# Kernel tuning notes

Hardware: AMD Instinct MI355X
Metric: run time of the kernel (lower is better)

## Reference

```python
import jax, jax.numpy as jnp
import numpy as np

D_MODEL = 1024
NUM_HEADS = 16
D_K = D_MODEL // NUM_HEADS


def setup_inputs() -> dict:
    key = jax.random.key(0)
    ks = jax.random.split(key, 11)
    B, S, D = 4, 2048, D_MODEL
    scale = 1.0 / np.sqrt(D)
    return {
        "Q": jax.random.normal(ks[0], (B, S, D), jnp.float32),
        "K": jax.random.normal(ks[1], (B, S, D), jnp.float32),
        "V": jax.random.normal(ks[2], (B, S, D), jnp.float32),
        "Wq": jax.random.normal(ks[3], (D, D), jnp.float32) * scale,
        "bq": jnp.zeros((D,), jnp.float32),
        "Wk": jax.random.normal(ks[4], (D, D), jnp.float32) * scale,
        "bk": jnp.zeros((D,), jnp.float32),
        "Wv": jax.random.normal(ks[5], (D, D), jnp.float32) * scale,
        "bv": jnp.zeros((D,), jnp.float32),
        "Wo": jax.random.normal(ks[6], (D, D), jnp.float32) * scale,
        "bo": jnp.zeros((D,), jnp.float32),
    }


def reference(Q, K, V, Wq, bq, Wk, bk, Wv, bv, Wo, bo):
    B, S, D = Q.shape
    H, Dk = NUM_HEADS, D_K
    # projections: [B,S,D] -> [B,H,S,Dk]
    def proj(x, W, b):
        y = jnp.einsum('bsd,de->bse', x, W.T) + b  # torch Linear: x @ W.T + b
        return y.reshape(B, -1, H, Dk).transpose(0, 2, 1, 3)
    q = proj(Q, Wq, bq)
    k = proj(K, Wk, bk)
    v = proj(V, Wv, bv)
    scores = jnp.einsum('bhqd,bhkd->bhqk', q, k) / np.sqrt(Dk)  # [B,H,S,S]
    attn = jax.nn.softmax(scores, axis=-1)
    out = jnp.einsum('bhqk,bhkd->bhqd', attn, v)  # [B,H,S,Dk]
    out = out.transpose(0, 2, 1, 3).reshape(B, -1, D)
    return jnp.einsum('bsd,de->bse', out, Wo.T) + bo
```

## Files before the change

kernel.cpp:

```cpp
#include <hip/hip_runtime.h>


typedef __bf16 bhalf_t;
typedef __attribute__((ext_vector_type(8)))  __bf16 bf16x8;
typedef __attribute__((ext_vector_type(4)))  __bf16 bf16x4;
typedef __attribute__((ext_vector_type(4)))  float  f32x4;
typedef __attribute__((ext_vector_type(16))) float  f32x16;

typedef __attribute__((address_space(1))) void gvoid_t;
typedef __attribute__((address_space(3))) void lvoid_t;
#define GLD16(g, l) __builtin_amdgcn_global_load_lds((const gvoid_t*)(g), (lvoid_t*)(l), 16, 0, 0)

__global__ __launch_bounds__(256) void cvt_all(
    const float* __restrict__ Q, const float* __restrict__ Kin, const float* __restrict__ V,
    const float* __restrict__ Wq, const float* __restrict__ Wk, const float* __restrict__ Wv,
    const float* __restrict__ Wo,
    bhalf_t* __restrict__ Qb, bhalf_t* __restrict__ Kb, bhalf_t* __restrict__ Vb,
    bhalf_t* __restrict__ Wqb, bhalf_t* __restrict__ Wkb, bhalf_t* __restrict__ Wvb,
    bhalf_t* __restrict__ Wob)
{
  size_t t = (size_t)blockIdx.x * 256 + threadIdx.x;
  const float* src; bhalf_t* dst;
  if (t < 2097152)      { src = Q;   dst = Qb; }
  else if (t < 4194304) { src = Kin; dst = Kb; t -= 2097152; }
  else if (t < 6291456) { src = V;   dst = Vb; t -= 4194304; }
  else {
    t -= 6291456;
    int w = (int)(t >> 18); t &= 262143;
    src = (w == 0) ? Wq  : (w == 1) ? Wk  : (w == 2) ? Wv  : Wo;
    dst = (w == 0) ? Wqb : (w == 1) ? Wkb : (w == 2) ? Wvb : Wob;
  }
  float4 f = ((const float4*)src)[t];
  bf16x4 o;
  o.x = (bhalf_t)f.x; o.y = (bhalf_t)f.y; o.z = (bhalf_t)f.z; o.w = (bhalf_t)f.w;
  ((bf16x4*)dst)[t] = o;
}

__device__ __forceinline__ void gemm_core_128(
    const bhalf_t* __restrict__ A, const bhalf_t* __restrict__ B,
    int bm, int bn, bhalf_t* As, bhalf_t* Bs, f32x4 acc[4][4])
{
  const int tid = threadIdx.x, lane = tid & 63, wave = tid >> 6;
  const int wm = wave >> 1, wn = wave & 1;
  const int quad = lane >> 4, tn = lane & 15;
  const int srow = lane >> 2, scol = (lane & 3) * 8;

  const bhalf_t* Ab0 = A + (size_t)(bm * 128 + wave * 16 + srow) * 1024 + scol;
  const bhalf_t* Ab1 = Ab0 + (size_t)64 * 1024;
  const bhalf_t* Bb0 = B + (size_t)(bn * 128 + wave * 16 + srow) * 1024 + scol;
  const bhalf_t* Bb1 = Bb0 + (size_t)64 * 1024;
  bhalf_t* Asw0 = As + wave * 512;  bhalf_t* Asw1 = As + (wave + 4) * 512;
  bhalf_t* Bsw0 = Bs + wave * 512;  bhalf_t* Bsw1 = Bs + (wave + 4) * 512;

  for (int k0 = 0; k0 < 1024; k0 += 32) {
    GLD16(Ab0 + k0, Asw0);
    GLD16(Ab1 + k0, Asw1);
    GLD16(Bb0 + k0, Bsw0);
    GLD16(Bb1 + k0, Bsw1);
    __syncthreads();
    bf16x8 af[4], bfr[4];
#pragma unroll
    for (int i = 0; i < 4; ++i)
      af[i] = *(const bf16x8*)(As + (wm * 64 + i * 16 + tn) * 32 + quad * 8);
#pragma unroll
    for (int j = 0; j < 4; ++j)
      bfr[j] = *(const bf16x8*)(Bs + (wn * 64 + j * 16 + tn) * 32 + quad * 8);
#pragma unroll
    for (int i = 0; i < 4; ++i)
#pragma unroll
      for (int j = 0; j < 4; ++j)
        acc[i][j] = __builtin_amdgcn_mfma_f32_16x16x32_bf16(af[i], bfr[j], acc[i][j], 0, 0, 0);
    __syncthreads();
  }
}

__global__ __launch_bounds__(256) void proj_gemm(
    const bhalf_t* __restrict__ Qb, const bhalf_t* __restrict__ Kb, const bhalf_t* __restrict__ Vb,
    const bhalf_t* __restrict__ Wqb, const bhalf_t* __restrict__ Wkb, const bhalf_t* __restrict__ Wvb,
    const float* __restrict__ bq, const float* __restrict__ bk, const float* __restrict__ bv,
    bhalf_t* __restrict__ qo, bhalf_t* __restrict__ ko, bhalf_t* __restrict__ vto)
{
  __shared__ bhalf_t As[4096];
  __shared__ bhalf_t Bs[4096];
  const int seg = blockIdx.x >> 9;
  const int idx = blockIdx.x & 511;
  const int bm = idx & 63, bn = idx >> 6;

  const bhalf_t *A, *Bw; const float* bias; bhalf_t* out; float scale; int mode;
  if (seg == 0)      { A = Qb; Bw = Wqb; bias = bq; out = qo;  scale = 0.18033688f; mode = 0; }
  else if (seg == 1) { A = Kb; Bw = Wkb; bias = bk; out = ko;  scale = 1.0f;        mode = 0; }
  else               { A = Vb; Bw = Wvb; bias = bv; out = vto; scale = 1.0f;        mode = 1; }

  f32x4 acc[4][4];
#pragma unroll
  for (int i = 0; i < 4; ++i)
#pragma unroll
    for (int j = 0; j < 4; ++j)
      acc[i][j] = (f32x4){0.f, 0.f, 0.f, 0.f};

  gemm_core_128(A, Bw, bm, bn, As, Bs, acc);

  const int lane = threadIdx.x & 63, wave = threadIdx.x >> 6;
  const int wm = wave >> 1, wn = wave & 1, quad = lane >> 4, tn = lane & 15;
#pragma unroll
  for (int i = 0; i < 4; ++i)
#pragma unroll
    for (int j = 0; j < 4; ++j) {
      const int n = bn * 128 + wn * 64 + j * 16 + tn;
      const float bsv = bias[n];
      const int h = n >> 6, dk = n & 63;
#pragma unroll
      for (int r = 0; r < 4; ++r) {
        const int m = bm * 128 + wm * 64 + i * 16 + quad * 4 + r;
        const int b = m >> 11, s = m & 2047;
        const float v = (acc[i][j][r] + bsv) * scale;
        size_t addr;
        if (mode == 0) addr = (((size_t)(b * 16 + h)) * 2048 + s) * 64 + dk;
        else {
          const int s2 = (s & ~12) | ((s & 4) << 1) | ((s & 8) >> 1);
          addr = (((size_t)(b * 16 + h)) * 64 + dk) * 2048 + s2;
        }
        out[addr] = (bhalf_t)v;
      }
    }
}

__global__ __launch_bounds__(256) void out_gemm(
    const bhalf_t* __restrict__ A, const bhalf_t* __restrict__ Bw,
    const float* __restrict__ bias, float* __restrict__ Cout)
{
  __shared__ bhalf_t As[4096];
  __shared__ bhalf_t Bs[4096];
  const int bm = blockIdx.x & 63, bn = blockIdx.x >> 6;

  f32x4 acc[4][4];
#pragma unroll
  for (int i = 0; i < 4; ++i)
#pragma unroll
    for (int j = 0; j < 4; ++j)
      acc[i][j] = (f32x4){0.f, 0.f, 0.f, 0.f};

  gemm_core_128(A, Bw, bm, bn, As, Bs, acc);

  const int lane = threadIdx.x & 63, wave = threadIdx.x >> 6;
  const int wm = wave >> 1, wn = wave & 1, quad = lane >> 4, tn = lane & 15;
#pragma unroll
  for (int i = 0; i < 4; ++i)
#pragma unroll
    for (int j = 0; j < 4; ++j) {
      const int n = bn * 128 + wn * 64 + j * 16 + tn;
      const float bsv = bias[n];
#pragma unroll
      for (int r = 0; r < 4; ++r) {
        const int m = bm * 128 + wm * 64 + i * 16 + quad * 4 + r;
        Cout[(size_t)m * 1024 + n] = acc[i][j][r] + bsv;
      }
    }
}

__global__ __launch_bounds__(256, 2) void attn_kernel(
    const bhalf_t* __restrict__ qp, const bhalf_t* __restrict__ kp,
    const bhalf_t* __restrict__ vtp, bhalf_t* __restrict__ outp)
{
  __shared__ bhalf_t Klds[4096];
  __shared__ bhalf_t Vtlds[4096];

  const int tid = threadIdx.x, lane = tid & 63, wave = tid >> 6;
  const int q31 = lane & 31, h = lane >> 5;
  const int bh = blockIdx.y, qt = blockIdx.x;

  const bhalf_t* qbase = qp + (((size_t)bh * 2048) + qt * 256 + wave * 64 + q31) * 64;
  bf16x8 qf[2][4];
#pragma unroll
  for (int qs = 0; qs < 2; ++qs)
#pragma unroll
    for (int ks = 0; ks < 4; ++ks)
      qf[qs][ks] = *(const bf16x8*)(qbase + qs * 32 * 64 + ks * 16 + h * 8);

  f32x16 Ot[2][2];
#pragma unroll
  for (int qs = 0; qs < 2; ++qs)
#pragma unroll
    for (int dd = 0; dd < 2; ++dd)
#pragma unroll
      for (int i = 0; i < 16; ++i) Ot[qs][dd][i] = 0.f;
  float Lp[2] = {0.f, 0.f};

  const bhalf_t* kbase  = kp  + (size_t)bh * 2048 * 64;
  const bhalf_t* vtbase = vtp + (size_t)bh * 64 * 2048;

  const int rloc = lane >> 3;
  const int cg8  = ((lane & 7) ^ rloc) * 8;
  const int q7 = q31 & 7;

  for (int kv0 = 0; kv0 < 2048; kv0 += 64) {
#pragma unroll
    for (int i = 0; i < 2; ++i) {
      const int r0 = (wave * 2 + i) * 8;
      GLD16(kbase + (size_t)(kv0 + r0 + rloc) * 64 + cg8, Klds + r0 * 64);
      GLD16(vtbase + (size_t)(r0 + rloc) * 2048 + kv0 + cg8, Vtlds + r0 * 64);
    }
    __syncthreads();

    bf16x8 pb[2][4];
#pragma unroll
    for (int mb = 0; mb < 2; ++mb) {
      bf16x8 ka[4];
#pragma unroll
      for (int ks = 0; ks < 4; ++ks)
        ka[ks] = *(const bf16x8*)(Klds + (mb * 32 + q31) * 64 + ((2 * ks + h) ^ q7) * 8);
#pragma unroll
      for (int qs = 0; qs < 2; ++qs) {
        f32x16 S;
#pragma unroll
        for (int i = 0; i < 16; ++i) S[i] = 0.f;
#pragma unroll
        for (int ks = 0; ks < 4; ++ks)
          S = __builtin_amdgcn_mfma_f32_32x32x16_bf16(ka[ks], qf[qs][ks], S, 0, 0, 0);
        float ls = 0.f;
#pragma unroll
        for (int half = 0; half < 2; ++half) {
          bf16x8 pk;
#pragma unroll
          for (int j = 0; j < 8; ++j) {
            const float e = __builtin_amdgcn_exp2f(S[half * 8 + j]);
            ls += e;
            pk[j] = (bhalf_t)e;
          }
          pb[qs][mb * 2 + half] = pk;
        }
        Lp[qs] += ls;
      }
    }

#pragma unroll
    for (int dd = 0; dd < 2; ++dd)
#pragma unroll
      for (int kb = 0; kb < 4; ++kb) {
        const bf16x8 va = *(const bf16x8*)(Vtlds + (dd * 32 + q31) * 64 + ((2 * kb + h) ^ q7) * 8);
#pragma unroll
        for (int qs = 0; qs < 2; ++qs)
          Ot[qs][dd] = __builtin_amdgcn_mfma_f32_32x32x16_bf16(va, pb[qs][kb], Ot[qs][dd], 0, 0, 0);
      }
    __syncthreads();
  }

  const int b = bh >> 4, hh = bh & 15;
#pragma unroll
  for (int qs = 0; qs < 2; ++qs) {
    const float Lt = Lp[qs] + __shfl_xor(Lp[qs], 32, 64);
    const float linv = 1.0f / Lt;
    const int s = qt * 256 + wave * 64 + qs * 32 + q31;
    bhalf_t* ob = outp + ((size_t)(b * 2048 + s)) * 1024 + hh * 64;
#pragma unroll
    for (int dd = 0; dd < 2; ++dd)
#pragma unroll
      for (int g = 0; g < 4; ++g) {
        bf16x4 o;
        o.x = (bhalf_t)(Ot[qs][dd][4 * g + 0] * linv);
        o.y = (bhalf_t)(Ot[qs][dd][4 * g + 1] * linv);
        o.z = (bhalf_t)(Ot[qs][dd][4 * g + 2] * linv);
        o.w = (bhalf_t)(Ot[qs][dd][4 * g + 3] * linv);
        *(bf16x4*)(ob + dd * 32 + g * 8 + h * 4) = o;
      }
  }
}

extern "C" void kernel_launch(void* const* d_in, const int* in_sizes, int n_in,
                              void* d_out, int out_size, void* d_ws, size_t ws_size,
                              hipStream_t stream)
{
  const float* Q  = (const float*)d_in[0];
  const float* K  = (const float*)d_in[1];
  const float* V  = (const float*)d_in[2];
  const float* Wq = (const float*)d_in[3];
  const float* bq = (const float*)d_in[4];
  const float* Wk = (const float*)d_in[5];
  const float* bk = (const float*)d_in[6];
  const float* Wv = (const float*)d_in[7];
  const float* bv = (const float*)d_in[8];
  const float* Wo = (const float*)d_in[9];
  const float* bo = (const float*)d_in[10];

  char* ws = (char*)d_ws;
  const size_t SZ = 8192ull * 1024 * 2;
  const size_t WZ = 1024ull * 1024 * 2;
  bhalf_t* Qb   = (bhalf_t*)(ws);
  bhalf_t* Kb   = (bhalf_t*)(ws + SZ);
  bhalf_t* Vb   = (bhalf_t*)(ws + 2 * SZ);
  bhalf_t* Wqb  = (bhalf_t*)(ws + 3 * SZ);
  bhalf_t* Wkb  = (bhalf_t*)(ws + 3 * SZ + WZ);
  bhalf_t* Wvb  = (bhalf_t*)(ws + 3 * SZ + 2 * WZ);
  bhalf_t* Wob  = (bhalf_t*)(ws + 3 * SZ + 3 * WZ);
  bhalf_t* q_p  = (bhalf_t*)(ws + 3 * SZ + 4 * WZ);
  bhalf_t* k_p  = (bhalf_t*)(ws + 4 * SZ + 4 * WZ);
  bhalf_t* vt_p = (bhalf_t*)(ws + 5 * SZ + 4 * WZ);
  bhalf_t* attn_o = Qb;

  cvt_all<<<28672, 256, 0, stream>>>(Q, K, V, Wq, Wk, Wv, Wo,
                                     Qb, Kb, Vb, Wqb, Wkb, Wvb, Wob);
  proj_gemm<<<1536, 256, 0, stream>>>(Qb, Kb, Vb, Wqb, Wkb, Wvb,
                                      bq, bk, bv, q_p, k_p, vt_p);
  attn_kernel<<<dim3(8, 64), 256, 0, stream>>>(q_p, k_p, vt_p, attn_o);
  out_gemm<<<512, 256, 0, stream>>>(attn_o, Wob, bo, (float*)d_out);
}
```

Baseline: 336.6 us.

## Rewrite projection GEMM as 256x256 tile with 4-stage async LDS pipeline

```diff
diff --git a/kernel.cpp b/kernel.cpp
--- a/kernel.cpp
+++ b/kernel.cpp
@@ -10,6 +10,11 @@
 typedef __attribute__((address_space(1))) void gvoid_t;
 typedef __attribute__((address_space(3))) void lvoid_t;
 #define GLD16(g, l) __builtin_amdgcn_global_load_lds((const gvoid_t*)(g), (lvoid_t*)(l), 16, 0, 0)
+
+#define SB0()   __builtin_amdgcn_sched_barrier(0)
+#define BARX()  asm volatile("s_barrier" ::: "memory")
+#define LGKM0() asm volatile("s_waitcnt lgkmcnt(0)" ::: "memory")
+#define VMW(n)  asm volatile("s_waitcnt vmcnt(" #n ")" ::: "memory")
 
 __global__ __launch_bounds__(256) void cvt_all(
     const float* __restrict__ Q, const float* __restrict__ Kin, const float* __restrict__ V,
@@ -74,44 +79,125 @@
   }
 }
 
-__global__ __launch_bounds__(256) void proj_gemm(
+#define PROJ_ITER(T, ISSUE, GATE)                                              \
+  {                                                                            \
+    bhalf_t* AsB = As + ((T) & 3) * 8192;                                      \
+    bhalf_t* BsB = Bs + ((T) & 3) * 8192;                                      \
+    bf16x8 af[4], bg[4];                                                       \
+    _Pragma("unroll")                                                          \
+    for (int i = 0; i < 4; ++i)                                                \
+      af[i] = *(const bf16x8*)(AsB + arow + i * 1024 + aswz);                  \
+    _Pragma("unroll")                                                          \
+    for (int j = 0; j < 4; ++j)                                                \
+      bg[j] = *(const bf16x8*)(BsB + brow + j * 1024 + bswz);                  \
+    if (ISSUE) {                                                               \
+      bhalf_t* And = As + (((T) + 3) & 3) * 8192;                              \
+      GLD16(Asrc0 + ((T) + 3) * 32, And + w * 512);                            \
+      GLD16(Asrc1 + ((T) + 3) * 32, And + (w + 8) * 512);                      \
+    }                                                                          \
+    BARX(); LGKM0(); SB0();                                                    \
+    __builtin_amdgcn_s_setprio(1);                                             \
+    _Pragma("unroll")                                                          \
+    for (int i = 0; i < 4; ++i)                                                \
+      _Pragma("unroll")                                                        \
+      for (int j = 0; j < 4; ++j)                                              \
+        acc[i][j] = __builtin_amdgcn_mfma_f32_16x16x32_bf16(af[i], bg[j], acc[i][j], 0, 0, 0); \
+    __builtin_amdgcn_s_setprio(0); SB0();                                      \
+    BARX();                                                                    \
+    _Pragma("unroll")                                                          \
+    for (int i = 0; i < 4; ++i)                                                \
+      af[i] = *(const bf16x8*)(AsB + arow + (i + 4) * 1024 + aswz);            \
+    if (ISSUE) {                                                               \
+      bhalf_t* Bnd = Bs + (((T) + 3) & 3) * 8192;                              \
+      GLD16(Bsrc0 + ((T) + 3) * 32, Bnd + w * 512);                            \
+      GLD16(Bsrc1 + ((T) + 3) * 32, Bnd + (w + 8) * 512);                      \
+    }                                                                          \
+    BARX(); LGKM0(); SB0();                                                    \
+    __builtin_amdgcn_s_setprio(1);                                             \
+    _Pragma("unroll")                                                          \
+    for (int i = 0; i < 4; ++i)                                                \
+      _Pragma("unroll")                                                        \
+      for (int j = 0; j < 4; ++j)                                              \
+        acc[i + 4][j] = __builtin_amdgcn_mfma_f32_16x16x32_bf16(af[i], bg[j], acc[i + 4][j], 0, 0, 0); \
+    __builtin_amdgcn_s_setprio(0); SB0();                                      \
+    GATE; SB0();                                                               \
+    BARX();                                                                    \
+  }
+
+__global__ __launch_bounds__(512, 2) void proj_gemm(
     const bhalf_t* __restrict__ Qb, const bhalf_t* __restrict__ Kb, const bhalf_t* __restrict__ Vb,
     const bhalf_t* __restrict__ Wqb, const bhalf_t* __restrict__ Wkb, const bhalf_t* __restrict__ Wvb,
     const float* __restrict__ bq, const float* __restrict__ bk, const float* __restrict__ bv,
     bhalf_t* __restrict__ qo, bhalf_t* __restrict__ ko, bhalf_t* __restrict__ vto)
 {
-  __shared__ bhalf_t As[4096];
-  __shared__ bhalf_t Bs[4096];
-  const int seg = blockIdx.x >> 9;
-  const int idx = blockIdx.x & 511;
-  const int bm = idx & 63, bn = idx >> 6;
+  __shared__ bhalf_t As[4 * 8192];
+  __shared__ bhalf_t Bs[4 * 8192];
+
+  const int bid = blockIdx.x;
+  const int wg = (bid & 7) * 48 + (bid >> 3);
+  const int seg = wg >> 7;
+  const int idx = wg & 127;
+  const int bm = idx >> 2, bn = idx & 3;
 
   const bhalf_t *A, *Bw; const float* bias; bhalf_t* out; float scale; int mode;
   if (seg == 0)      { A = Qb; Bw = Wqb; bias = bq; out = qo;  scale = 0.18033688f; mode = 0; }
   else if (seg == 1) { A = Kb; Bw = Wkb; bias = bk; out = ko;  scale = 1.0f;        mode = 0; }
   else               { A = Vb; Bw = Wvb; bias = bv; out = vto; scale = 1.0f;        mode = 1; }
 
-  f32x4 acc[4][4];
-#pragma unroll
-  for (int i = 0; i < 4; ++i)
+  const int tid = threadIdx.x, lane = tid & 63, w = tid >> 6;
+  const int wm = w >> 2, wn = w & 3;
+  const int quad = lane >> 4, tn = lane & 15;
+
+  const int c    = (lane & 7) ^ ((lane >> 3) & 7);
+  const int rA   = w * 8 + (lane >> 3);
+  const int grow = rA + 128 * (c >> 2);
+  const int kcol = (c & 3) * 8;
+  const bhalf_t* Asrc0 = A  + (size_t)(bm * 256 + grow) * 1024 + kcol;
+  const bhalf_t* Asrc1 = Asrc0 + (size_t)64 * 1024;
+  const bhalf_t* Bsrc0 = Bw + (size_t)(bn * 256 + grow) * 1024 + kcol;
+  const bhalf_t* Bsrc1 = Bsrc0 + (size_t)64 * 1024;
+
+  const int aswz = (((wm << 2) | quad) ^ (tn & 7)) * 8;
+  const int bswz = ((((wn >> 1) << 2) | quad) ^ (tn & 7)) * 8;
+  const int arow = tn * 64;
+  const int brow = (((wn & 1) << 6) + tn) * 64;
+
+  f32x4 acc[8][4];
+#pragma unroll
+  for (int i = 0; i < 8; ++i)
 #pragma unroll
     for (int j = 0; j < 4; ++j)
       acc[i][j] = (f32x4){0.f, 0.f, 0.f, 0.f};
 
-  gemm_core_128(A, Bw, bm, bn, As, Bs, acc);
-
-  const int lane = threadIdx.x & 63, wave = threadIdx.x >> 6;
-  const int wm = wave >> 1, wn = wave & 1, quad = lane >> 4, tn = lane & 15;
-#pragma unroll
-  for (int i = 0; i < 4; ++i)
+#pragma unroll
+  for (int t = 0; t < 3; ++t) {
+    bhalf_t* And = As + t * 8192;
+    bhalf_t* Bnd = Bs + t * 8192;
+    GLD16(Asrc0 + t * 32, And + w * 512);
+    GLD16(Asrc1 + t * 32, And + (w + 8) * 512);
+    GLD16(Bsrc0 + t * 32, Bnd + w * 512);
+    GLD16(Bsrc1 + t * 32, Bnd + (w + 8) * 512);
+  }
+  VMW(8); SB0();
+  BARX();
+
+#pragma unroll 4
+  for (int t = 0; t < 28; ++t) PROJ_ITER(t, true, VMW(8));
+  PROJ_ITER(28, true,  VMW(8));
+  PROJ_ITER(29, false, VMW(4));
+  PROJ_ITER(30, false, VMW(0));
+  PROJ_ITER(31, false, (void)0);
+
+#pragma unroll
+  for (int i = 0; i < 8; ++i)
 #pragma unroll
     for (int j = 0; j < 4; ++j) {
-      const int n = bn * 128 + wn * 64 + j * 16 + tn;
+      const int n = bn * 256 + wn * 64 + j * 16 + tn;
       const float bsv = bias[n];
       const int h = n >> 6, dk = n & 63;
 #pragma unroll
       for (int r = 0; r < 4; ++r) {
-        const int m = bm * 128 + wm * 64 + i * 16 + quad * 4 + r;
+        const int m = bm * 256 + wm * 128 + i * 16 + quad * 4 + r;
         const int b = m >> 11, s = m & 2047;
         const float v = (acc[i][j][r] + bsv) * scale;
         size_t addr;
@@ -299,8 +385,8 @@
 
   cvt_all<<<28672, 256, 0, stream>>>(Q, K, V, Wq, Wk, Wv, Wo,
                                      Qb, Kb, Vb, Wqb, Wkb, Wvb, Wob);
-  proj_gemm<<<1536, 256, 0, stream>>>(Qb, Kb, Vb, Wqb, Wkb, Wvb,
-                                      bq, bk, bv, q_p, k_p, vt_p);
+  proj_gemm<<<384, 512, 0, stream>>>(Qb, Kb, Vb, Wqb, Wkb, Wvb,
+                                     bq, bk, bv, q_p, k_p, vt_p);
   attn_kernel<<<dim3(8, 64), 256, 0, stream>>>(q_p, k_p, vt_p, attn_o);
   out_gemm<<<512, 256, 0, stream>>>(attn_o, Wob, bo, (float*)d_out);
 }
```

Result: slower. 366.3 us (+8.8%).

## Fuse fp32-to-bf16 activation conversion into projection GEMM and swizzle LDS tiles

Applied to the files above, without the earlier changes.

```diff
diff --git a/kernel.cpp b/kernel.cpp
--- a/kernel.cpp
+++ b/kernel.cpp
@@ -11,60 +11,57 @@
 typedef __attribute__((address_space(3))) void lvoid_t;
 #define GLD16(g, l) __builtin_amdgcn_global_load_lds((const gvoid_t*)(g), (lvoid_t*)(l), 16, 0, 0)
 
-__global__ __launch_bounds__(256) void cvt_all(
-    const float* __restrict__ Q, const float* __restrict__ Kin, const float* __restrict__ V,
-    const float* __restrict__ Wq, const float* __restrict__ Wk, const float* __restrict__ Wv,
-    const float* __restrict__ Wo,
-    bhalf_t* __restrict__ Qb, bhalf_t* __restrict__ Kb, bhalf_t* __restrict__ Vb,
-    bhalf_t* __restrict__ Wqb, bhalf_t* __restrict__ Wkb, bhalf_t* __restrict__ Wvb,
-    bhalf_t* __restrict__ Wob)
+__global__ __launch_bounds__(256) void cvt_w(
+    const float* __restrict__ Wq, const float* __restrict__ Wk,
+    const float* __restrict__ Wv, const float* __restrict__ Wo,
+    bhalf_t* __restrict__ Wqb, bhalf_t* __restrict__ Wkb,
+    bhalf_t* __restrict__ Wvb, bhalf_t* __restrict__ Wob)
 {
   size_t t = (size_t)blockIdx.x * 256 + threadIdx.x;
-  const float* src; bhalf_t* dst;
-  if (t < 2097152)      { src = Q;   dst = Qb; }
-  else if (t < 4194304) { src = Kin; dst = Kb; t -= 2097152; }
-  else if (t < 6291456) { src = V;   dst = Vb; t -= 4194304; }
-  else {
-    t -= 6291456;
-    int w = (int)(t >> 18); t &= 262143;
-    src = (w == 0) ? Wq  : (w == 1) ? Wk  : (w == 2) ? Wv  : Wo;
-    dst = (w == 0) ? Wqb : (w == 1) ? Wkb : (w == 2) ? Wvb : Wob;
-  }
+  int w = (int)(t >> 18); t &= 262143;
+  const float* src = (w == 0) ? Wq  : (w == 1) ? Wk  : (w == 2) ? Wv  : Wo;
+  bhalf_t*     dst = (w == 0) ? Wqb : (w == 1) ? Wkb : (w == 2) ? Wvb : Wob;
   float4 f = ((const float4*)src)[t];
   bf16x4 o;
   o.x = (bhalf_t)f.x; o.y = (bhalf_t)f.y; o.z = (bhalf_t)f.z; o.w = (bhalf_t)f.w;
   ((bf16x4*)dst)[t] = o;
 }
 
-__device__ __forceinline__ void gemm_core_128(
+__device__ __forceinline__ void gemm_core_128_swz(
     const bhalf_t* __restrict__ A, const bhalf_t* __restrict__ B,
     int bm, int bn, bhalf_t* As, bhalf_t* Bs, f32x4 acc[4][4])
 {
   const int tid = threadIdx.x, lane = tid & 63, wave = tid >> 6;
   const int wm = wave >> 1, wn = wave & 1;
   const int quad = lane >> 4, tn = lane & 15;
-  const int srow = lane >> 2, scol = (lane & 3) * 8;
-
-  const bhalf_t* Ab0 = A + (size_t)(bm * 128 + wave * 16 + srow) * 1024 + scol;
-  const bhalf_t* Ab1 = Ab0 + (size_t)64 * 1024;
-  const bhalf_t* Bb0 = B + (size_t)(bn * 128 + wave * 16 + srow) * 1024 + scol;
-  const bhalf_t* Bb1 = Bb0 + (size_t)64 * 1024;
-  bhalf_t* Asw0 = As + wave * 512;  bhalf_t* Asw1 = As + (wave + 4) * 512;
-  bhalf_t* Bsw0 = Bs + wave * 512;  bhalf_t* Bsw1 = Bs + (wave + 4) * 512;
+
+  const int u    = (lane & 7) ^ (lane >> 3);
+  const int roff = (lane >> 3) + 64 * (u >> 2);
+  const int gk   = (u & 3) * 8;
+
+  const bhalf_t* Ag0 = A + (size_t)(bm * 128 + wave * 8 + roff) * 1024 + gk;
+  const bhalf_t* Ag1 = A + (size_t)(bm * 128 + (wave + 4) * 8 + roff) * 1024 + gk;
+  const bhalf_t* Bg0 = B + (size_t)(bn * 128 + wave * 8 + roff) * 1024 + gk;
+  const bhalf_t* Bg1 = B + (size_t)(bn * 128 + (wave + 4) * 8 + roff) * 1024 + gk;
+  bhalf_t* Ad0 = As + wave * 512;  bhalf_t* Ad1 = As + (wave + 4) * 512;
+  bhalf_t* Bd0 = Bs + wave * 512;  bhalf_t* Bd1 = Bs + (wave + 4) * 512;
+
+  const int aswz = ((wm * 4 + quad) ^ (tn & 7)) * 8;
+  const int bswz = ((wn * 4 + quad) ^ (tn & 7)) * 8;
 
   for (int k0 = 0; k0 < 1024; k0 += 32) {
-    GLD16(Ab0 + k0, Asw0);
-    GLD16(Ab1 + k0, Asw1);
-    GLD16(Bb0 + k0, Bsw0);
-    GLD16(Bb1 + k0, Bsw1);
+    GLD16(Ag0 + k0, Ad0);
+    GLD16(Ag1 + k0, Ad1);
+    GLD16(Bg0 + k0, Bd0);
+    GLD16(Bg1 + k0, Bd1);
     __syncthreads();
     bf16x8 af[4], bfr[4];
 #pragma unroll
     for (int i = 0; i < 4; ++i)
-      af[i] = *(const bf16x8*)(As + (wm * 64 + i * 16 + tn) * 32 + quad * 8);
+      af[i] = *(const bf16x8*)(As + (i * 16 + tn) * 64 + aswz);
 #pragma unroll
     for (int j = 0; j < 4; ++j)
-      bfr[j] = *(const bf16x8*)(Bs + (wn * 64 + j * 16 + tn) * 32 + quad * 8);
+      bfr[j] = *(const bf16x8*)(Bs + (j * 16 + tn) * 64 + bswz);
 #pragma unroll
     for (int i = 0; i < 4; ++i)
 #pragma unroll
@@ -75,7 +72,7 @@
 }
 
 __global__ __launch_bounds__(256) void proj_gemm(
-    const bhalf_t* __restrict__ Qb, const bhalf_t* __restrict__ Kb, const bhalf_t* __restrict__ Vb,
+    const float* __restrict__ Qf, const float* __restrict__ Kf, const float* __restrict__ Vf,
     const bhalf_t* __restrict__ Wqb, const bhalf_t* __restrict__ Wkb, const bhalf_t* __restrict__ Wvb,
     const float* __restrict__ bq, const float* __restrict__ bk, const float* __restrict__ bv,
     bhalf_t* __restrict__ qo, bhalf_t* __restrict__ ko, bhalf_t* __restrict__ vto)
@@ -86,10 +83,30 @@
   const int idx = blockIdx.x & 511;
   const int bm = idx & 63, bn = idx >> 6;
 
-  const bhalf_t *A, *Bw; const float* bias; bhalf_t* out; float scale; int mode;
-  if (seg == 0)      { A = Qb; Bw = Wqb; bias = bq; out = qo;  scale = 0.18033688f; mode = 0; }
-  else if (seg == 1) { A = Kb; Bw = Wkb; bias = bk; out = ko;  scale = 1.0f;        mode = 0; }
-  else               { A = Vb; Bw = Wvb; bias = bv; out = vto; scale = 1.0f;        mode = 1; }
+  const float *A; const bhalf_t *Bw; const float* bias; bhalf_t* out; float scale; int mode;
+  if (seg == 0)      { A = Qf; Bw = Wqb; bias = bq; out = qo;  scale = 0.18033688f; mode = 0; }
+  else if (seg == 1) { A = Kf; Bw = Wkb; bias = bk; out = ko;  scale = 1.0f;        mode = 0; }
+  else               { A = Vf; Bw = Wvb; bias = bv; out = vto; scale = 1.0f;        mode = 1; }
+
+  const int tid = threadIdx.x, lane = tid & 63, wave = tid >> 6;
+  const int wm = wave >> 1, wn = wave & 1;
+  const int quad = lane >> 4, tn = lane & 15;
+
+  const int u    = (lane & 7) ^ (lane >> 3);
+  const int roff = (lane >> 3) + 64 * (u >> 2);
+  const int gk   = (u & 3) * 8;
+
+  const float* Af0 = A + (size_t)(bm * 128 + wave * 8 + roff) * 1024 + gk;
+  const float* Af1 = A + (size_t)(bm * 128 + (wave + 4) * 8 + roff) * 1024 + gk;
+  bhalf_t* Ad0 = As + wave * 512 + lane * 8;
+  bhalf_t* Ad1 = As + (wave + 4) * 512 + lane * 8;
+  const bhalf_t* Bg0 = Bw + (size_t)(bn * 128 + wave * 8 + roff) * 1024 + gk;
+  const bhalf_t* Bg1 = Bw + (size_t)(bn * 128 + (wave + 4) * 8 + roff) * 1024 + gk;
+  bhalf_t* Bd0 = Bs + wave * 512;
+  bhalf_t* Bd1 = Bs + (wave + 4) * 512;
+
+  const int aswz = ((wm * 4 + quad) ^ (tn & 7)) * 8;
+  const int bswz = ((wn * 4 + quad) ^ (tn & 7)) * 8;
 
   f32x4 acc[4][4];
 #pragma unroll
@@ -98,10 +115,40 @@
     for (int j = 0; j < 4; ++j)
       acc[i][j] = (f32x4){0.f, 0.f, 0.f, 0.f};
 
-  gemm_core_128(A, Bw, bm, bn, As, Bs, acc);
-
-  const int lane = threadIdx.x & 63, wave = threadIdx.x >> 6;
-  const int wm = wave >> 1, wn = wave & 1, quad = lane >> 4, tn = lane & 15;
+  for (int k0 = 0; k0 < 1024; k0 += 32) {
+    GLD16(Bg0 + k0, Bd0);
+    GLD16(Bg1 + k0, Bd1);
+    float4 a00 = *(const float4*)(Af0 + k0);
+    float4 a01 = *(const float4*)(Af0 + k0 + 4);
+    float4 a10 = *(const float4*)(Af1 + k0);
+    float4 a11 = *(const float4*)(Af1 + k0 + 4);
+    bf16x8 v0, v1;
+    v0[0] = (bhalf_t)a00.x; v0[1] = (bhalf_t)a00.y;
+    v0[2] = (bhalf_t)a00.z; v0[3] = (bhalf_t)a00.w;
+    v0[4] = (bhalf_t)a01.x; v0[5] = (bhalf_t)a01.y;
+    v0[6] = (bhalf_t)a01.z; v0[7] = (bhalf_t)a01.w;
+    v1[0] = (bhalf_t)a10.x; v1[1] = (bhalf_t)a10.y;
+    v1[2] = (bhalf_t)a10.z; v1[3] = (bhalf_t)a10.w;
+    v1[4] = (bhalf_t)a11.x; v1[5] = (bhalf_t)a11.y;
+    v1[6] = (bhalf_t)a11.z; v1[7] = (bhalf_t)a11.w;
+    *(bf16x8*)Ad0 = v0;
+    *(bf16x8*)Ad1 = v1;
+    __syncthreads();
+    bf16x8 af[4], bfr[4];
+#pragma unroll
+    for (int i = 0; i < 4; ++i)
+      af[i] = *(const bf16x8*)(As + (i * 16 + tn) * 64 + aswz);
+#pragma unroll
+    for (int j = 0; j < 4; ++j)
+      bfr[j] = *(const bf16x8*)(Bs + (j * 16 + tn) * 64 + bswz);
+#pragma unroll
+    for (int i = 0; i < 4; ++i)
+#pragma unroll
+      for (int j = 0; j < 4; ++j)
+        acc[i][j] = __builtin_amdgcn_mfma_f32_16x16x32_bf16(af[i], bfr[j], acc[i][j], 0, 0, 0);
+    __syncthreads();
+  }
+
 #pragma unroll
   for (int i = 0; i < 4; ++i)
 #pragma unroll
@@ -140,7 +187,7 @@
     for (int j = 0; j < 4; ++j)
       acc[i][j] = (f32x4){0.f, 0.f, 0.f, 0.f};
 
-  gemm_core_128(A, Bw, bm, bn, As, Bs, acc);
+  gemm_core_128_swz(A, Bw, bm, bn, As, Bs, acc);
 
   const int lane = threadIdx.x & 63, wave = threadIdx.x >> 6;
   const int wm = wave >> 1, wn = wave & 1, quad = lane >> 4, tn = lane & 15;
@@ -285,21 +332,17 @@
   char* ws = (char*)d_ws;
   const size_t SZ = 8192ull * 1024 * 2;
   const size_t WZ = 1024ull * 1024 * 2;
-  bhalf_t* Qb   = (bhalf_t*)(ws);
-  bhalf_t* Kb   = (bhalf_t*)(ws + SZ);
-  bhalf_t* Vb   = (bhalf_t*)(ws + 2 * SZ);
-  bhalf_t* Wqb  = (bhalf_t*)(ws + 3 * SZ);
-  bhalf_t* Wkb  = (bhalf_t*)(ws + 3 * SZ + WZ);
-  bhalf_t* Wvb  = (bhalf_t*)(ws + 3 * SZ + 2 * WZ);
-  bhalf_t* Wob  = (bhalf_t*)(ws + 3 * SZ + 3 * WZ);
-  bhalf_t* q_p  = (bhalf_t*)(ws + 3 * SZ + 4 * WZ);
-  bhalf_t* k_p  = (bhalf_t*)(ws + 4 * SZ + 4 * WZ);
-  bhalf_t* vt_p = (bhalf_t*)(ws + 5 * SZ + 4 * WZ);
-  bhalf_t* attn_o = Qb;
-
-  cvt_all<<<28672, 256, 0, stream>>>(Q, K, V, Wq, Wk, Wv, Wo,
-                                     Qb, Kb, Vb, Wqb, Wkb, Wvb, Wob);
-  proj_gemm<<<1536, 256, 0, stream>>>(Qb, Kb, Vb, Wqb, Wkb, Wvb,
+  bhalf_t* Wqb  = (bhalf_t*)(ws);
+  bhalf_t* Wkb  = (bhalf_t*)(ws + WZ);
+  bhalf_t* Wvb  = (bhalf_t*)(ws + 2 * WZ);
+  bhalf_t* Wob  = (bhalf_t*)(ws + 3 * WZ);
+  bhalf_t* q_p  = (bhalf_t*)(ws + 4 * WZ);
+  bhalf_t* k_p  = (bhalf_t*)(ws + 4 * WZ + SZ);
+  bhalf_t* vt_p = (bhalf_t*)(ws + 4 * WZ + 2 * SZ);
+  bhalf_t* attn_o = (bhalf_t*)(ws + 4 * WZ + 3 * SZ);
+
+  cvt_w<<<4096, 256, 0, stream>>>(Wq, Wk, Wv, Wo, Wqb, Wkb, Wvb, Wob);
+  proj_gemm<<<1536, 256, 0, stream>>>(Q, K, V, Wqb, Wkb, Wvb,
                                       bq, bk, bv, q_p, k_p, vt_p);
   attn_kernel<<<dim3(8, 64), 256, 0, stream>>>(q_p, k_p, vt_p, attn_o);
   out_gemm<<<512, 256, 0, stream>>>(attn_o, Wob, bo, (float*)d_out);
```

After: 356.2 us. 1.06x slower.
